# Kernel tuning notes

Hardware: AMD Instinct MI355X
Metric: run time of the kernel (lower is better)

The kernel has to match this reference:

```python
import jax, jax.numpy as jnp
import numpy as np

VOCAB = 128000
SEED = 0
PRIOR_TOKENS = 4
DEPTH = 16
TOP_P = 0.9


def setup_inputs() -> dict:
    key = jax.random.key(0)
    k1, k2 = jax.random.split(key)
    input_ids = jax.random.randint(k1, (32, 2048), 0, VOCAB, dtype=jnp.int64 if jax.config.jax_enable_x64 else jnp.int32)
    logits = jax.random.normal(k2, (32, VOCAB), dtype=jnp.float32)
    return {"input_ids": input_ids, "logits": logits}


def _g_values(prior_ids, depth, vocab):
    # Faithful structure: a deterministic Bernoulli(0.5) table of shape [B, depth, vocab]
    # seeded by (seed, prior_ids[b], depth_index). The original uses sha256+numpy RNG;
    # here we use the idiomatic JAX counterpart (fold_in keyed PRNG).
    base = jax.random.key(SEED)
    d_idx = jnp.arange(depth)

    def per_depth(k_b, i):
        return jax.random.bernoulli(jax.random.fold_in(k_b, i), 0.5, (vocab,))

    def per_batch(p):
        k_b = jax.random.fold_in(base, p.astype(jnp.uint32))
        return jax.vmap(lambda i: per_depth(k_b, i))(d_idx)

    return jax.vmap(per_batch)(prior_ids).astype(jnp.float32)  # [B, depth, V]


def _top_p_sample(probs_b, key, top_p):
    V = probs_b.shape[-1]
    sorted_probs, sorted_idx = jax.lax.top_k(probs_b, V)  # descending
    cum = jnp.cumsum(sorted_probs)
    cutoff = jnp.searchsorted(cum, top_p, side='left')
    keep = jnp.arange(V) <= cutoff  # zero out indices > cutoff (matches [cutoff+1:] = 0)
    sp = jnp.where(keep, sorted_probs, 0.0)
    sp = sp / sp.sum()
    sp = jnp.where(jnp.isfinite(sp), sp, 0.0)
    tok = jax.random.categorical(key, jnp.log(sp))  # multinomial(1)
    return sorted_idx[tok]


def reference(input_ids, logits):
    B, V = logits.shape
    prior_ids = input_ids[:, -PRIOR_TOKENS:].sum(axis=-1)  # [B]
    g = _g_values(prior_ids, DEPTH, V)                     # [B, depth, V]

    probs = jax.nn.softmax(logits, axis=-1)
    for i in range(DEPTH):
        g_i = g[:, i, :]                                   # [B, V]
        g_mass = jnp.sum(g_i * probs, axis=-1, keepdims=True)
        probs = probs * (1.0 + g_i - g_mass)

    sample_keys = jax.random.split(jax.random.key(SEED + 1), B)
    next_tokens = jax.vmap(lambda p, k: _top_p_sample(p, k, TOP_P))(probs, sample_keys)

    scores = jnp.full_like(logits, 1e-05)
    scores = scores.at[jnp.arange(B), next_tokens].set(100000.0)
    return scores
```

## Files before the change

kernel.cpp:

```cpp
#include <hip/hip_runtime.h>
#include <stdint.h>


#define NB 32
#define NV 128000
#define NDEPTH 16
#define NTB 500
#define NCB 125
#define NBINS 512
#define CAP 96256
#define NBLKH 94
#define FPSCALE 17592186044416.0
#define TSCALE  68719476736.0
#define MSCALE 1.152921504606846976e18

typedef unsigned long long u64;

__device__ __forceinline__ uint32_t rotl32(uint32_t v, int r) {
  return __builtin_amdgcn_alignbit(v, v, (32 - r) & 31);
}

__device__ __forceinline__ void tf2x32(uint32_t k0, uint32_t k1,
                                       uint32_t x0, uint32_t x1,
                                       uint32_t &o0, uint32_t &o1) {
  uint32_t ks2 = k0 ^ k1 ^ 0x1BD11BDAu;
  x0 += k0; x1 += k1;
  x0 += x1; x1 = rotl32(x1, 13); x1 ^= x0;
  x0 += x1; x1 = rotl32(x1, 15); x1 ^= x0;
  x0 += x1; x1 = rotl32(x1, 26); x1 ^= x0;
  x0 += x1; x1 = rotl32(x1,  6); x1 ^= x0;
  x0 += k1; x1 += ks2 + 1u;
  x0 += x1; x1 = rotl32(x1, 17); x1 ^= x0;
  x0 += x1; x1 = rotl32(x1, 29); x1 ^= x0;
  x0 += x1; x1 = rotl32(x1, 16); x1 ^= x0;
  x0 += x1; x1 = rotl32(x1, 24); x1 ^= x0;
  x0 += ks2; x1 += k0 + 2u;
  x0 += x1; x1 = rotl32(x1, 13); x1 ^= x0;
  x0 += x1; x1 = rotl32(x1, 15); x1 ^= x0;
  x0 += x1; x1 = rotl32(x1, 26); x1 ^= x0;
  x0 += x1; x1 = rotl32(x1,  6); x1 ^= x0;
  x0 += k0; x1 += k1 + 3u;
  x0 += x1; x1 = rotl32(x1, 17); x1 ^= x0;
  x0 += x1; x1 = rotl32(x1, 29); x1 ^= x0;
  x0 += x1; x1 = rotl32(x1, 16); x1 ^= x0;
  x0 += x1; x1 = rotl32(x1, 24); x1 ^= x0;
  x0 += k1; x1 += ks2 + 4u;
  x0 += x1; x1 = rotl32(x1, 13); x1 ^= x0;
  x0 += x1; x1 = rotl32(x1, 15); x1 ^= x0;
  x0 += x1; x1 = rotl32(x1, 26); x1 ^= x0;
  x0 += x1; x1 = rotl32(x1,  6); x1 ^= x0;
  x0 += ks2; x1 += k0 + 5u;
  o0 = x0; o1 = x1;
}

__device__ __forceinline__ uint32_t random_bits32(uint32_t k0, uint32_t k1, uint32_t i) {
  uint32_t y0, y1;
  tf2x32(k0, k1, 0u, i, y0, y1);
  return y0 ^ y1;
}

__global__ void keys_k(const int* __restrict__ ids, int T,
                       uint32_t* __restrict__ kd, uint32_t* __restrict__ sk) {
  int t = threadIdx.x;
  if (t >= NB) return;
  uint32_t prior = 0;
  for (int q = 0; q < 4; ++q) prior += (uint32_t)ids[(size_t)t * T + (T - 4) + q];
  uint32_t b0, b1;
  tf2x32(0u, 0u, 0u, prior, b0, b1);
  for (int d = 0; d < NDEPTH; ++d) {
    uint32_t y0, y1;
    tf2x32(b0, b1, 0u, (uint32_t)d, y0, y1);
    kd[(t * NDEPTH + d) * 2 + 0] = y0;
    kd[(t * NDEPTH + d) * 2 + 1] = y1;
  }
  uint32_t s0, s1;
  tf2x32(0u, 1u, 0u, (uint32_t)t, s0, s1);
  sk[2 * t + 0] = s0;
  sk[2 * t + 1] = s1;
}

__global__ void gmaskmax_k(const uint32_t* __restrict__ kd, const float* __restrict__ logits,
                           uint16_t* __restrict__ mask, float* __restrict__ pmax) {
  int blk = blockIdx.x, t = threadIdx.x;
  int b = blk / NTB, c = blk % NTB;
  uint32_t v = (uint32_t)(c * 256 + t);
  size_t i = (size_t)b * NV + v;
  const uint32_t* kp = kd + b * NDEPTH * 2;
  uint32_t m = 0;
  #pragma unroll
  for (int d = NDEPTH - 1; d >= 0; --d) {
    uint32_t k0 = __builtin_amdgcn_readfirstlane(kp[2 * d]);
    uint32_t k1 = __builtin_amdgcn_readfirstlane(kp[2 * d + 1]);
    uint32_t bits = random_bits32(k0, k1, v);
    m = (m << 1) | (bits >> 31);
  }
  mask[i] = (uint16_t)(m ^ 0xFFFFu);
  float x = logits[i];
  for (int o = 32; o > 0; o >>= 1) x = fmaxf(x, __shfl_xor(x, o));
  __shared__ float wmax[4];
  if ((t & 63) == 0) wmax[t >> 6] = x;
  __syncthreads();
  if (t == 0) pmax[b * NTB + c] = fmaxf(fmaxf(wmax[0], wmax[1]), fmaxf(wmax[2], wmax[3]));
}

__global__ void maxr2_k(const float* __restrict__ pmax, float* __restrict__ mx) {
  int t = threadIdx.x;
  int b = t >> 5, k = t & 31;
  float m = -3.4e38f;
  for (int i = k; i < NTB; i += 32) m = fmaxf(m, pmax[b * NTB + i]);
  for (int o = 16; o > 0; o >>= 1) m = fmaxf(m, __shfl_xor(m, o, 32));
  if (k == 0) mx[b] = m;
}

__global__ void lohist_k(const float* __restrict__ logits, const uint16_t* __restrict__ mask,
                         const float* __restrict__ mx, float* __restrict__ ef,
                         u64* __restrict__ Hlo) {
  int blk = blockIdx.x, t = threadIdx.x;
  int b = blk / NCB, c = blk % NCB;
  __shared__ u64 h[256];
  h[t] = 0ull;
  __syncthreads();
  float mxb = mx[b];
  size_t base = (size_t)b * NV + (size_t)c * 1024;
  #pragma unroll
  for (int e = 0; e < 4; ++e) {
    size_t i = base + e * 256 + t;
    float x = expf(logits[i] - mxb);
    ef[i] = x;
    atomicAdd(&h[mask[i] & 255u], (u64)((double)x * FPSCALE));
  }
  __syncthreads();
  if (h[t]) atomicAdd(&Hlo[b * 256 + t], h[t]);
}

__global__ void faclo_k(const u64* __restrict__ Hlo, u64* __restrict__ Zint,
                        float* __restrict__ zf, float* __restrict__ gm,
                        float* __restrict__ wloTab) {
  int b = blockIdx.x, t = threadIdx.x;
  u64 v = Hlo[b * 256 + t];
  __shared__ u64 zr[256];
  zr[t] = v; __syncthreads();
  for (int s = 128; s > 0; s >>= 1) { if (t < s) zr[t] += zr[t + s]; __syncthreads(); }
  __shared__ double Zsh;
  if (t == 0) {
    Zint[b] = zr[0];
    Zsh = (double)zr[0] * (1.0 / FPSCALE);
    zf[b] = (float)Zsh;
  }
  __syncthreads();
  double Zd = Zsh;
  float base = (float)((double)v * (1.0 / FPSCALE) / Zd);
  float w = 1.0f;
  __shared__ double dr[256];
  for (int d = 0; d < 8; ++d) {
    int bit = (t >> d) & 1;
    dr[t] = bit ? (double)(base * w) : 0.0;
    __syncthreads();
    for (int s = 128; s > 0; s >>= 1) { if (t < s) dr[t] += dr[t + s]; __syncthreads(); }
    float g = (float)dr[0];
    if (t == 0) gm[b * NDEPTH + d] = g;
    w *= (1.0f + (float)bit) - g;
    __syncthreads();
  }
  wloTab[b * 256 + t] = w;
}

__global__ void hihist_k(const float* __restrict__ ef, const uint16_t* __restrict__ mask,
                         const float* __restrict__ wloTab, u64* __restrict__ Thist) {
  int blk = blockIdx.x, t = threadIdx.x;
  int b = blk / NCB, c = blk % NCB;
  __shared__ u64 h[256];
  __shared__ float wl[256];
  h[t] = 0ull;
  wl[t] = wloTab[b * 256 + t];
  __syncthreads();
  size_t base = (size_t)b * NV + (size_t)c * 1024;
  #pragma unroll
  for (int e = 0; e < 4; ++e) {
    size_t i = base + e * 256 + t;
    uint32_t mk = mask[i];
    double prod = (double)ef[i] * (double)wl[mk & 255u];
    atomicAdd(&h[mk >> 8], (u64)(prod * TSCALE));
  }
  __syncthreads();
  if (h[t]) atomicAdd(&Thist[b * 256 + t], h[t]);
}

__global__ void fachi_k(const u64* __restrict__ Thist, const u64* __restrict__ Zint,
                        float* __restrict__ gm) {
  int b = blockIdx.x, t = threadIdx.x;
  double Zd = (double)Zint[b] * (1.0 / FPSCALE);
  u64 v = Thist[b * 256 + t];
  float base = (float)((double)v * (1.0 / TSCALE) / Zd);
  float w = 1.0f;
  __shared__ double dr[256];
  for (int d = 8; d < NDEPTH; ++d) {
    int bit = (t >> (d - 8)) & 1;
    dr[t] = bit ? (double)(base * w) : 0.0;
    __syncthreads();
    for (int s = 128; s > 0; s >>= 1) { if (t < s) dr[t] += dr[t + s]; __syncthreads(); }
    float g = (float)dr[0];
    if (t == 0) gm[b * NDEPTH + d] = g;
    w *= (1.0f + (float)bit) - g;
    __syncthreads();
  }
}

__global__ void final_k(float* __restrict__ efkeys, const uint16_t* __restrict__ mask,
                        const float* __restrict__ zf, const float* __restrict__ gm,
                        u64* __restrict__ binmass, uint32_t* __restrict__ bincnt) {
  int blk = blockIdx.x, t = threadIdx.x;
  int b = blk / NCB, c = blk % NCB;
  __shared__ float gsh[NDEPTH];
  __shared__ float zsh;
  __shared__ u64 bm[NBINS];
  __shared__ uint32_t bc[NBINS];
  if (t < NDEPTH) gsh[t] = gm[b * NDEPTH + t];
  if (t == 16) zsh = zf[b];
  for (int i = t; i < NBINS; i += 256) { bm[i] = 0ull; bc[i] = 0u; }
  __syncthreads();
  size_t base = (size_t)b * NV + (size_t)c * 1024;
  #pragma unroll
  for (int e = 0; e < 4; ++e) {
    size_t i = base + e * 256 + t;
    float p = efkeys[i] / zsh;
    uint16_t mk = mask[i];
    #pragma unroll
    for (int d = 0; d < NDEPTH; ++d) {
      float g = (float)((mk >> d) & 1);
      p = p * ((1.0f + g) - gsh[d]);
    }
    uint32_t key = ~__float_as_uint(p);
    ((uint32_t*)efkeys)[i] = key;
    uint32_t bin = key >> 23;
    atomicAdd(&bm[bin], (u64)((double)p * MSCALE));
    atomicAdd(&bc[bin], 1u);
  }
  __syncthreads();
  for (int k = t; k < NBINS; k += 256) {
    if (bc[k]) atomicAdd(&bincnt[b * NBINS + k], bc[k]);
    if (bm[k]) atomicAdd(&binmass[b * NBINS + k], bm[k]);
  }
}

__launch_bounds__(512)
__global__ void binsel_k(const u64* __restrict__ binmass, const uint32_t* __restrict__ bincnt,
                         uint32_t* __restrict__ Kthr, uint32_t* __restrict__ Hlen) {
  int b = blockIdx.x, t = threadIdx.x;
  __shared__ u64 cm[NBINS];
  __shared__ uint32_t cc[NBINS];
  __shared__ int selB;
  cm[t] = binmass[b * NBINS + t];
  cc[t] = bincnt[b * NBINS + t];
  if (t == 0) selB = NBINS - 2;
  __syncthreads();
  for (int off = 1; off < NBINS; off <<= 1) {
    u64 a = (t >= off) ? cm[t - off] : 0ull;
    uint32_t d = (t >= off) ? cc[t - off] : 0u;
    __syncthreads();
    cm[t] += a; cc[t] += d;
    __syncthreads();
  }
  const u64 thr = (u64)((double)0.9f * MSCALE);
  if (cm[t] >= thr && (t == 0 || cm[t - 1] < thr)) atomicMin(&selB, t);
  __syncthreads();
  if (t == 0) {
    int sb = selB;
    int margin = (cm[sb] >= thr && (cm[sb] - thr) > (1ull << 22)) ? 0 : 1;
    int Bs = sb + margin;
    if (Bs > NBINS - 1) Bs = NBINS - 1;
    while (Bs > 0 && cc[Bs] > CAP) --Bs;
    u64 kt = (((u64)(Bs + 1)) << 23) - 1ull;
    Kthr[b] = (uint32_t)kt;
    Hlen[b] = cc[Bs];
  }
}

__global__ void hcount_k(const uint32_t* __restrict__ keys, const uint32_t* __restrict__ Kthr,
                         uint32_t* __restrict__ hcnt) {
  int blk = blockIdx.x, t = threadIdx.x;
  int b = blk / NTB, c = blk % NTB;
  size_t i = (size_t)blk * 256 + t;
  bool active = keys[i] <= Kthr[b];
  u64 am = __ballot(active);
  __shared__ uint32_t wc[4];
  if ((t & 63) == 0) wc[t >> 6] = (uint32_t)__popcll(am);
  __syncthreads();
  if (t == 0) hcnt[b * NTB + c] = wc[0] + wc[1] + wc[2] + wc[3];
}

__launch_bounds__(1024)
__global__ void hscan_k(uint32_t* __restrict__ hcnt) {
  int b = blockIdx.x, t = threadIdx.x;
  uint32_t v = (t < NTB) ? hcnt[b * NTB + t] : 0u;
  __shared__ uint32_t sc[1024];
  sc[t] = v;
  __syncthreads();
  for (int off = 1; off < 1024; off <<= 1) {
    uint32_t a = (t >= off) ? sc[t - off] : 0u;
    __syncthreads();
    sc[t] += a;
    __syncthreads();
  }
  if (t < NTB) hcnt[b * NTB + t] = sc[t] - v;
}

__global__ void hcompact_k(const uint32_t* __restrict__ keys, const uint32_t* __restrict__ Kthr,
                           const uint32_t* __restrict__ hcnt, uint2* __restrict__ headA) {
  int blk = blockIdx.x, t = threadIdx.x;
  int b = blk / NTB, c = blk % NTB;
  int v = c * 256 + t;
  size_t i = (size_t)blk * 256 + t;
  uint32_t key = keys[i];
  bool active = key <= Kthr[b];
  int w = t >> 6, lane = t & 63;
  u64 am = __ballot(active);
  uint32_t rank = (uint32_t)__popcll(am & ((1ull << lane) - 1ull));
  __shared__ uint32_t wc[4];
  if ((t & 63) == 0) wc[t >> 6] = (uint32_t)__popcll(am);
  __syncthreads();
  uint32_t off = hcnt[b * NTB + c] + rank;
  for (int w2 = 0; w2 < w; ++w2) off += wc[w2];
  if (active) headA[(size_t)b * CAP + off] = make_uint2(key, (uint32_t)v);
}

__global__ void rhist_k(const uint2* __restrict__ src, const uint32_t* __restrict__ Hlen,
                        uint32_t* __restrict__ cnt, int shift) {
  int blk = blockIdx.x, t = threadIdx.x;
  int b = blk / NBLKH, c = blk % NBLKH;
  uint32_t H = Hlen[b];
  if ((uint32_t)(c * 1024) >= H) { cnt[((size_t)b * 256 + t) * NBLKH + c] = 0u; return; }
  const uint2* s = src + (size_t)b * CAP + (size_t)c * 1024;
  __shared__ uint32_t lh[256];
  lh[t] = 0;
  __syncthreads();
  #pragma unroll
  for (int e = 0; e < 4; ++e) {
    uint32_t idx = (uint32_t)(c * 1024 + 256 * e + t);
    if (idx < H) atomicAdd(&lh[(s[t + 256 * e].x >> shift) & 255u], 1u);
  }
  __syncthreads();
  cnt[((size_t)b * 256 + t) * NBLKH + c] = lh[t];
}

__launch_bounds__(1024)
__global__ void rscan_k(uint32_t* __restrict__ cnt) {
  const int NE = 256 * NBLKH;
  const int NL = 24;
  int b = blockIdx.x, t = threadIdx.x;
  uint32_t* cc = cnt + (size_t)b * NE;
  uint32_t loc[NL];
  uint32_t s = 0;
  int base = t * NL;
  #pragma unroll
  for (int j = 0; j < NL; ++j) {
    loc[j] = (base + j < NE) ? cc[base + j] : 0u;
    s += loc[j];
  }
  __shared__ uint32_t sc[1024];
  sc[t] = s;
  __syncthreads();
  for (int off = 1; off < 1024; off <<= 1) {
    uint32_t v = (t >= off) ? sc[t - off] : 0u;
    __syncthreads();
    sc[t] += v;
    __syncthreads();
  }
  uint32_t run = sc[t] - s;
  #pragma unroll
  for (int j = 0; j < NL; ++j) {
    if (base + j < NE) { uint32_t o = loc[j]; cc[base + j] = run; run += o; }
  }
}

__launch_bounds__(256)
__global__ void rscatter_k(const uint2* __restrict__ src, uint2* __restrict__ dst,
                           const uint32_t* __restrict__ Hlen,
                           const uint32_t* __restrict__ cnt, int shift) {
  int blk = blockIdx.x, t = threadIdx.x;
  int b = blk / NBLKH, c = blk % NBLKH;
  uint32_t H = Hlen[b];
  if ((uint32_t)(c * 1024) >= H) return;
  const uint2* s = src + (size_t)b * CAP + (size_t)c * 1024;
  uint2* d = dst + (size_t)b * CAP;
  int w = t >> 6, lane = t & 63;
  __shared__ uint32_t runb[256];
  __shared__ uint32_t wvc[4][256];
  runb[t] = cnt[((size_t)b * 256 + t) * NBLKH + c];
  uint2 el[4];
  #pragma unroll
  for (int e = 0; e < 4; ++e) el[e] = s[t + 256 * e];
  u64 lowmask = (1ull << lane) - 1ull;
  #pragma unroll
  for (int e = 0; e < 4; ++e) {
    uint32_t* wf = &wvc[0][0];
    wf[t] = 0; wf[t + 256] = 0; wf[t + 512] = 0; wf[t + 768] = 0;
    __syncthreads();
    bool active = (uint32_t)(c * 1024 + 256 * e + t) < H;
    uint32_t dig = active ? ((el[e].x >> shift) & 255u) : 0u;
    u64 act = __ballot(active);
    u64 m = ~0ull;
    #pragma unroll
    for (int bit = 0; bit < 8; ++bit) {
      u64 bb = __ballot((dig >> bit) & 1u);
      m &= ((dig >> bit) & 1u) ? bb : ~bb;
    }
    m &= act;
    uint32_t rank = (uint32_t)__popcll(m & lowmask);
    if (active && rank == 0) wvc[w][dig] = (uint32_t)__popcll(m);
    __syncthreads();
    if (active) {
      uint32_t off = runb[dig] + rank;
      for (int w2 = 0; w2 < w; ++w2) off += wvc[w2][dig];
      d[off] = el[e];
    }
    __syncthreads();
    runb[t] += wvc[0][t] + wvc[1][t] + wvc[2][t] + wvc[3][t];
    __syncthreads();
  }
}

__global__ void chunks_k(const uint2* __restrict__ sp, const uint32_t* __restrict__ Hlen,
                         double* __restrict__ cs) {
  int blk = blockIdx.x, t = threadIdx.x;
  int b = blk / NBLKH, c = blk % NBLKH;
  uint32_t H = Hlen[b];
  if ((uint32_t)(c * 1024) >= H) { if (t == 0) cs[b * NBLKH + c] = 0.0; return; }
  const uint2* p = sp + (size_t)b * CAP + (size_t)c * 1024;
  double s = 0.0;
  for (int k = t; k < 1024; k += 256) {
    uint32_t idx = (uint32_t)(c * 1024 + k);
    if (idx < H) s += (double)__uint_as_float(~p[k].x);
  }
  __shared__ double red[256];
  red[t] = s; __syncthreads();
  for (int st = 128; st > 0; st >>= 1) {
    if (t < st) red[t] += red[t + st];
    __syncthreads();
  }
  if (t == 0) cs[b * NBLKH + c] = red[0];
}

__launch_bounds__(1024)
__global__ void cutargmax_k(const uint2* __restrict__ sp, const double* __restrict__ cs,
                            const uint32_t* __restrict__ Hlen,
                            const uint32_t* __restrict__ sk, u64* __restrict__ best) {
  int b = blockIdx.x, t = threadIdx.x;
  const double TOPP = (double)0.9f;
  uint32_t H = Hlen[b];
  __shared__ double scd[1024];
  __shared__ int chSel;
  __shared__ double baseSel;
  __shared__ uint32_t cutSh;
  if (t == 0) { chSel = -1; baseSel = 0.0; cutSh = H - 1; }
  double v = (t < NBLKH) ? cs[b * NBLKH + t] : 0.0;
  scd[t] = v;
  __syncthreads();
  for (int off = 1; off < 1024; off <<= 1) {
    double a = (t >= off) ? scd[t - off] : 0.0;
    __syncthreads();
    scd[t] += a;
    __syncthreads();
  }
  if (t < NBLKH && scd[t] >= TOPP && (t == 0 || scd[t - 1] < TOPP)) {
    chSel = t;
    baseSel = (t == 0) ? 0.0 : scd[t - 1];
  }
  __syncthreads();
  int CH = chSel;
  if (CH >= 0) {
    double base = baseSel;
    uint32_t idx = (uint32_t)(CH * 1024 + t);
    double pv = (idx < H) ? (double)__uint_as_float(~sp[(size_t)b * CAP + idx].x) : 0.0;
    __syncthreads();
    scd[t] = pv;
    __syncthreads();
    for (int off = 1; off < 1024; off <<= 1) {
      double a = (t >= off) ? scd[t - off] : 0.0;
      __syncthreads();
      scd[t] += a;
      __syncthreads();
    }
    __shared__ int kSel;
    if (t == 0) kSel = 1023;
    __syncthreads();
    if (base + scd[t] >= TOPP && (t == 0 || base + scd[t - 1] < TOPP)) kSel = t;
    __syncthreads();
    if (t == 0) cutSh = (uint32_t)(CH * 1024 + kSel);
  }
  __syncthreads();
  uint32_t c = cutSh;
  uint32_t k0 = sk[2 * b], k1 = sk[2 * b + 1];
  u64 loc = 0ull;
  for (uint32_t j = (uint32_t)t; j <= c; j += 1024) {
    uint32_t bits = random_bits32(k0, k1, j);
    uint32_t m = bits >> 9;
    float u = (m == 0u) ? 1.17549435e-38f : (float)m * 1.1920928955078125e-7f;
    float gum = -logf(-logf(u));
    float scv = logf(__uint_as_float(~sp[(size_t)b * CAP + j].x)) + gum;
    uint32_t su = __float_as_uint(scv);
    uint32_t ord = (su & 0x80000000u) ? ~su : (su | 0x80000000u);
    u64 pk = ((u64)ord << 32) | (u64)(0xFFFFFFFFu - j);
    loc = (pk > loc) ? pk : loc;
  }
  __shared__ u64 redm[1024];
  redm[t] = loc;
  __syncthreads();
  for (int st = 512; st > 0; st >>= 1) {
    if (t < st) {
      u64 o = redm[t + st];
      if (o > redm[t]) redm[t] = o;
    }
    __syncthreads();
  }
  if (t == 0) best[b] = redm[0];
}

__global__ void fill_k(float* __restrict__ out) {
  size_t i = (size_t)blockIdx.x * 256 + threadIdx.x;
  out[i] = 1e-5f;
}

__global__ void win_k(const u64* __restrict__ best, const uint2* __restrict__ sp,
                      float* __restrict__ out) {
  int b = threadIdx.x;
  if (b >= NB) return;
  u64 pk = best[b];
  uint32_t j = 0xFFFFFFFFu - (uint32_t)(pk & 0xFFFFFFFFull);
  uint32_t tok = sp[(size_t)b * CAP + j].y;
  out[(size_t)b * NV + tok] = 100000.0f;
}

extern "C" void kernel_launch(void* const* d_in, const int* in_sizes, int n_in,
                              void* d_out, int out_size, void* d_ws, size_t ws_size,
                              hipStream_t stream) {
  const int* ids = (const int*)d_in[0];
  const float* logits = (const float*)d_in[1];
  float* out = (float*)d_out;
  int T = in_sizes[0] / NB;

  char* w = (char*)d_ws;
  uint2*    headA = (uint2*)(w + 0);
  uint2*    headB = (uint2*)(w + 24641536);
  uint16_t* mask  = (uint16_t*)(w + 49283072);
  float*    efkeys = (float*)(w + 24641536);
  uint32_t* keys   = (uint32_t*)(w + 24641536);
  uint32_t* cnt    = (uint32_t*)(w + 49283072);
  double*   csum   = (double*)(w + 52400000);
  char* S = w + 57475072;
  float*    pmax    = (float*)(S + 0);
  uint32_t* hcnt    = (uint32_t*)(S + 64000);
  float*    mx      = (float*)(S + 128000);
  float*    zf      = (float*)(S + 128128);
  float*    gm      = (float*)(S + 128256);
  uint32_t* kd      = (uint32_t*)(S + 130304);
  uint32_t* sk      = (uint32_t*)(S + 134400);
  u64*      best    = (u64*)(S + 134656);
  uint32_t* Kthr    = (uint32_t*)(S + 134912);
  uint32_t* Hlen    = (uint32_t*)(S + 135040);
  u64*      Zint    = (u64*)(S + 135168);
  float*    wloTab  = (float*)(S + 135424);
  char* ZR = S + 168192;
  u64*      Hlo     = (u64*)(ZR + 0);
  u64*      Thist   = (u64*)(ZR + 65536);
  u64*      binmass = (u64*)(ZR + 131072);
  uint32_t* bincnt  = (uint32_t*)(ZR + 262144);

  const int BVBLK = NB * NTB;
  const int CBLK  = NB * NCB;

  hipMemsetAsync(ZR, 0, 327680, stream);
  keys_k<<<1, 64, 0, stream>>>(ids, T, kd, sk);
  gmaskmax_k<<<BVBLK, 256, 0, stream>>>(kd, logits, mask, pmax);
  maxr2_k<<<1, 1024, 0, stream>>>(pmax, mx);
  lohist_k<<<CBLK, 256, 0, stream>>>(logits, mask, mx, efkeys, Hlo);
  faclo_k<<<NB, 256, 0, stream>>>(Hlo, Zint, zf, gm, wloTab);
  hihist_k<<<CBLK, 256, 0, stream>>>(efkeys, mask, wloTab, Thist);
  fachi_k<<<NB, 256, 0, stream>>>(Thist, Zint, gm);
  final_k<<<CBLK, 256, 0, stream>>>(efkeys, mask, zf, gm, binmass, bincnt);
  binsel_k<<<NB, NBINS, 0, stream>>>(binmass, bincnt, Kthr, Hlen);
  hcount_k<<<BVBLK, 256, 0, stream>>>(keys, Kthr, hcnt);
  hscan_k<<<NB, 1024, 0, stream>>>(hcnt);
  hcompact_k<<<BVBLK, 256, 0, stream>>>(keys, Kthr, hcnt, headA);

  const uint2* srcs[4] = { headA, headB, headA, headB };
  uint2*       dsts[4] = { headB, headA, headB, headA };
  for (int pass = 0; pass < 4; ++pass) {
    int shift = pass * 8;
    rhist_k<<<NB * NBLKH, 256, 0, stream>>>(srcs[pass], Hlen, cnt, shift);
    rscan_k<<<NB, 1024, 0, stream>>>(cnt);
    rscatter_k<<<NB * NBLKH, 256, 0, stream>>>(srcs[pass], dsts[pass], Hlen, cnt, shift);
  }

  chunks_k<<<NB * NBLKH, 256, 0, stream>>>(headA, Hlen, csum);
  cutargmax_k<<<NB, 1024, 0, stream>>>(headA, csum, Hlen, sk, best);
  fill_k<<<BVBLK, 256, 0, stream>>>(out);
  win_k<<<1, 32, 0, stream>>>(best, headA, out);
}
```

Baseline: 438.8 us.

## Fuse compaction into first radix pass, recompute exp, use wave-level scans

Several independent changes land together. The first radix pass now reads keys directly and filters them by threshold, which replaces the separate count/scan/compact kernels and removes one full radix pass. The exp(logit - max) values are recomputed in each kernel instead of being stored and reloaded, and the zeroing memset is folded into gmaskmax. Shared-memory Hillis-Steele scans and reductions in faclo, fachi, binsel, rscan and cutargmax become shuffle-based wave scans. This trades extra transcendental work and extra kernel complexity for fewer launches, passes and barriers.

```diff
diff --git a/kernel.cpp b/kernel.cpp
--- a/kernel.cpp
+++ b/kernel.cpp
@@ -80,19 +80,24 @@
 }
 
 __global__ void gmaskmax_k(const uint32_t* __restrict__ kd, const float* __restrict__ logits,
-                           uint16_t* __restrict__ mask, float* __restrict__ pmax) {
-  int blk = blockIdx.x, t = threadIdx.x;
+                           uint16_t* __restrict__ mask, float* __restrict__ pmax,
+                           uint32_t* __restrict__ ZR) {
+  int blk = blockIdx.x, t = threadIdx.x;
+  if (blk < 320) ZR[blk * 256 + t] = 0u;
   int b = blk / NTB, c = blk % NTB;
+  uint32_t K0[NDEPTH], K1[NDEPTH];
+  #pragma unroll
+  for (int d = 0; d < NDEPTH; ++d) {
+    K0[d] = kd[b * NDEPTH * 2 + 2 * d];
+    K1[d] = kd[b * NDEPTH * 2 + 2 * d + 1];
+  }
   uint32_t v = (uint32_t)(c * 256 + t);
   size_t i = (size_t)b * NV + v;
-  const uint32_t* kp = kd + b * NDEPTH * 2;
   uint32_t m = 0;
   #pragma unroll
   for (int d = NDEPTH - 1; d >= 0; --d) {
-    uint32_t k0 = __builtin_amdgcn_readfirstlane(kp[2 * d]);
-    uint32_t k1 = __builtin_amdgcn_readfirstlane(kp[2 * d + 1]);
-    uint32_t bits = random_bits32(k0, k1, v);
-    m = (m << 1) | (bits >> 31);
+    uint32_t bits = random_bits32(K0[d], K1[d], v);
+    m = __builtin_amdgcn_alignbit(m, bits, 31);
   }
   mask[i] = (uint16_t)(m ^ 0xFFFFu);
   float x = logits[i];
@@ -113,8 +118,7 @@
 }
 
 __global__ void lohist_k(const float* __restrict__ logits, const uint16_t* __restrict__ mask,
-                         const float* __restrict__ mx, float* __restrict__ ef,
-                         u64* __restrict__ Hlo) {
+                         const float* __restrict__ mx, u64* __restrict__ Hlo) {
   int blk = blockIdx.x, t = threadIdx.x;
   int b = blk / NCB, c = blk % NCB;
   __shared__ u64 h[256];
@@ -126,7 +130,6 @@
   for (int e = 0; e < 4; ++e) {
     size_t i = base + e * 256 + t;
     float x = expf(logits[i] - mxb);
-    ef[i] = x;
     atomicAdd(&h[mask[i] & 255u], (u64)((double)x * FPSCALE));
   }
   __syncthreads();
@@ -136,37 +139,42 @@
 __global__ void faclo_k(const u64* __restrict__ Hlo, u64* __restrict__ Zint,
                         float* __restrict__ zf, float* __restrict__ gm,
                         float* __restrict__ wloTab) {
-  int b = blockIdx.x, t = threadIdx.x;
-  u64 v = Hlo[b * 256 + t];
-  __shared__ u64 zr[256];
-  zr[t] = v; __syncthreads();
-  for (int s = 128; s > 0; s >>= 1) { if (t < s) zr[t] += zr[t + s]; __syncthreads(); }
-  __shared__ double Zsh;
-  if (t == 0) {
-    Zint[b] = zr[0];
-    Zsh = (double)zr[0] * (1.0 / FPSCALE);
-    zf[b] = (float)Zsh;
-  }
-  __syncthreads();
-  double Zd = Zsh;
-  float base = (float)((double)v * (1.0 / FPSCALE) / Zd);
-  float w = 1.0f;
-  __shared__ double dr[256];
+  int b = blockIdx.x, l = threadIdx.x;
+  u64 v[4];
+  #pragma unroll
+  for (int q = 0; q < 4; ++q) v[q] = Hlo[b * 256 + l + 64 * q];
+  u64 zp = v[0] + v[1] + v[2] + v[3];
+  for (int o = 32; o > 0; o >>= 1) zp += __shfl_xor(zp, o);
+  double Zd = (double)zp * (1.0 / FPSCALE);
+  if (l == 0) { Zint[b] = zp; zf[b] = (float)Zd; }
+  float base[4], w[4];
+  #pragma unroll
+  for (int q = 0; q < 4; ++q) {
+    base[q] = (float)((double)v[q] * (1.0 / FPSCALE) / Zd);
+    w[q] = 1.0f;
+  }
+  #pragma unroll
   for (int d = 0; d < 8; ++d) {
-    int bit = (t >> d) & 1;
-    dr[t] = bit ? (double)(base * w) : 0.0;
-    __syncthreads();
-    for (int s = 128; s > 0; s >>= 1) { if (t < s) dr[t] += dr[t + s]; __syncthreads(); }
-    float g = (float)dr[0];
-    if (t == 0) gm[b * NDEPTH + d] = g;
-    w *= (1.0f + (float)bit) - g;
-    __syncthreads();
-  }
-  wloTab[b * 256 + t] = w;
-}
-
-__global__ void hihist_k(const float* __restrict__ ef, const uint16_t* __restrict__ mask,
-                         const float* __restrict__ wloTab, u64* __restrict__ Thist) {
+    double part = 0.0;
+    #pragma unroll
+    for (int q = 0; q < 4; ++q)
+      if (((l + 64 * q) >> d) & 1) part += (double)(base[q] * w[q]);
+    for (int o = 32; o > 0; o >>= 1) part += __shfl_xor(part, o);
+    float g = (float)part;
+    if (l == 0) gm[b * NDEPTH + d] = g;
+    #pragma unroll
+    for (int q = 0; q < 4; ++q) {
+      int bit = ((l + 64 * q) >> d) & 1;
+      w[q] *= (1.0f + (float)bit) - g;
+    }
+  }
+  #pragma unroll
+  for (int q = 0; q < 4; ++q) wloTab[b * 256 + l + 64 * q] = w[q];
+}
+
+__global__ void hihist_k(const float* __restrict__ logits, const uint16_t* __restrict__ mask,
+                         const float* __restrict__ mx, const float* __restrict__ wloTab,
+                         u64* __restrict__ Thist) {
   int blk = blockIdx.x, t = threadIdx.x;
   int b = blk / NCB, c = blk % NCB;
   __shared__ u64 h[256];
@@ -174,12 +182,14 @@
   h[t] = 0ull;
   wl[t] = wloTab[b * 256 + t];
   __syncthreads();
+  float mxb = mx[b];
   size_t base = (size_t)b * NV + (size_t)c * 1024;
   #pragma unroll
   for (int e = 0; e < 4; ++e) {
     size_t i = base + e * 256 + t;
+    float x = expf(logits[i] - mxb);
     uint32_t mk = mask[i];
-    double prod = (double)ef[i] * (double)wl[mk & 255u];
+    double prod = (double)x * (double)wl[mk & 255u];
     atomicAdd(&h[mk >> 8], (u64)(prod * TSCALE));
   }
   __syncthreads();
@@ -188,42 +198,54 @@
 
 __global__ void fachi_k(const u64* __restrict__ Thist, const u64* __restrict__ Zint,
                         float* __restrict__ gm) {
-  int b = blockIdx.x, t = threadIdx.x;
+  int b = blockIdx.x, l = threadIdx.x;
   double Zd = (double)Zint[b] * (1.0 / FPSCALE);
-  u64 v = Thist[b * 256 + t];
-  float base = (float)((double)v * (1.0 / TSCALE) / Zd);
-  float w = 1.0f;
-  __shared__ double dr[256];
+  u64 v[4];
+  #pragma unroll
+  for (int q = 0; q < 4; ++q) v[q] = Thist[b * 256 + l + 64 * q];
+  float base[4], w[4];
+  #pragma unroll
+  for (int q = 0; q < 4; ++q) {
+    base[q] = (float)((double)v[q] * (1.0 / TSCALE) / Zd);
+    w[q] = 1.0f;
+  }
+  #pragma unroll
   for (int d = 8; d < NDEPTH; ++d) {
-    int bit = (t >> (d - 8)) & 1;
-    dr[t] = bit ? (double)(base * w) : 0.0;
-    __syncthreads();
-    for (int s = 128; s > 0; s >>= 1) { if (t < s) dr[t] += dr[t + s]; __syncthreads(); }
-    float g = (float)dr[0];
-    if (t == 0) gm[b * NDEPTH + d] = g;
-    w *= (1.0f + (float)bit) - g;
-    __syncthreads();
-  }
-}
-
-__global__ void final_k(float* __restrict__ efkeys, const uint16_t* __restrict__ mask,
-                        const float* __restrict__ zf, const float* __restrict__ gm,
+    double part = 0.0;
+    #pragma unroll
+    for (int q = 0; q < 4; ++q)
+      if (((l + 64 * q) >> (d - 8)) & 1) part += (double)(base[q] * w[q]);
+    for (int o = 32; o > 0; o >>= 1) part += __shfl_xor(part, o);
+    float g = (float)part;
+    if (l == 0) gm[b * NDEPTH + d] = g;
+    #pragma unroll
+    for (int q = 0; q < 4; ++q) {
+      int bit = ((l + 64 * q) >> (d - 8)) & 1;
+      w[q] *= (1.0f + (float)bit) - g;
+    }
+  }
+}
+
+__global__ void final_k(const float* __restrict__ logits, const uint16_t* __restrict__ mask,
+                        const float* __restrict__ mx, const float* __restrict__ zf,
+                        const float* __restrict__ gm, uint32_t* __restrict__ keys,
                         u64* __restrict__ binmass, uint32_t* __restrict__ bincnt) {
   int blk = blockIdx.x, t = threadIdx.x;
   int b = blk / NCB, c = blk % NCB;
   __shared__ float gsh[NDEPTH];
-  __shared__ float zsh;
+  __shared__ float zsh, msh;
   __shared__ u64 bm[NBINS];
   __shared__ uint32_t bc[NBINS];
   if (t < NDEPTH) gsh[t] = gm[b * NDEPTH + t];
   if (t == 16) zsh = zf[b];
+  if (t == 17) msh = mx[b];
   for (int i = t; i < NBINS; i += 256) { bm[i] = 0ull; bc[i] = 0u; }
   __syncthreads();
   size_t base = (size_t)b * NV + (size_t)c * 1024;
   #pragma unroll
   for (int e = 0; e < 4; ++e) {
     size_t i = base + e * 256 + t;
-    float p = efkeys[i] / zsh;
+    float p = expf(logits[i] - msh) / zsh;
     uint16_t mk = mask[i];
     #pragma unroll
     for (int d = 0; d < NDEPTH; ++d) {
@@ -231,7 +253,7 @@
       p = p * ((1.0f + g) - gsh[d]);
     }
     uint32_t key = ~__float_as_uint(p);
-    ((uint32_t*)efkeys)[i] = key;
+    keys[i] = key;
     uint32_t bin = key >> 23;
     atomicAdd(&bm[bin], (u64)((double)p * MSCALE));
     atomicAdd(&bc[bin], 1u);
@@ -243,85 +265,152 @@
   }
 }
 
-__launch_bounds__(512)
 __global__ void binsel_k(const u64* __restrict__ binmass, const uint32_t* __restrict__ bincnt,
                          uint32_t* __restrict__ Kthr, uint32_t* __restrict__ Hlen) {
-  int b = blockIdx.x, t = threadIdx.x;
-  __shared__ u64 cm[NBINS];
-  __shared__ uint32_t cc[NBINS];
-  __shared__ int selB;
-  cm[t] = binmass[b * NBINS + t];
-  cc[t] = bincnt[b * NBINS + t];
-  if (t == 0) selB = NBINS - 2;
-  __syncthreads();
-  for (int off = 1; off < NBINS; off <<= 1) {
-    u64 a = (t >= off) ? cm[t - off] : 0ull;
-    uint32_t d = (t >= off) ? cc[t - off] : 0u;
-    __syncthreads();
-    cm[t] += a; cc[t] += d;
-    __syncthreads();
-  }
+  int b = blockIdx.x, l = threadIdx.x;
+  u64 m[8]; uint32_t c[8];
+  #pragma unroll
+  for (int r = 0; r < 8; ++r) {
+    m[r] = binmass[b * NBINS + l * 8 + r];
+    c[r] = bincnt[b * NBINS + l * 8 + r];
+  }
+  #pragma unroll
+  for (int r = 1; r < 8; ++r) { m[r] += m[r - 1]; c[r] += c[r - 1]; }
+  u64 lm = m[7]; uint32_t lc = c[7];
+  u64 im = lm; uint32_t ic = lc;
+  for (int o = 1; o < 64; o <<= 1) {
+    u64 nm = __shfl_up(im, o);
+    uint32_t nc = __shfl_up(ic, o);
+    if (l >= o) { im += nm; ic += nc; }
+  }
+  u64 baseM = im - lm;
+  uint32_t baseC = ic - lc;
+  __shared__ uint32_t ccL[NBINS];
+  #pragma unroll
+  for (int r = 0; r < 8; ++r) ccL[l * 8 + r] = baseC + c[r];
   const u64 thr = (u64)((double)0.9f * MSCALE);
-  if (cm[t] >= thr && (t == 0 || cm[t - 1] < thr)) atomicMin(&selB, t);
-  __syncthreads();
-  if (t == 0) {
-    int sb = selB;
-    int margin = (cm[sb] >= thr && (cm[sb] - thr) > (1ull << 22)) ? 0 : 1;
-    int Bs = sb + margin;
+  int localFirst = 8; u64 cmAt = 0ull;
+  #pragma unroll
+  for (int r = 0; r < 8; ++r) {
+    if (localFirst == 8 && baseM + m[r] >= thr) { localFirst = r; cmAt = baseM + m[r]; }
+  }
+  u64 bal = __ballot(localFirst < 8);
+  int selB = NBINS - 2; u64 cmSel = 0ull;
+  if (bal) {
+    int fl = __ffsll((unsigned long long)bal) - 1;
+    int sl = __shfl(localFirst, fl);
+    cmSel = __shfl(cmAt, fl);
+    selB = fl * 8 + sl;
+  }
+  __syncthreads();
+  if (l == 0) {
+    int margin = (cmSel >= thr && (cmSel - thr) > (1ull << 22)) ? 0 : 1;
+    int Bs = selB + margin;
     if (Bs > NBINS - 1) Bs = NBINS - 1;
-    while (Bs > 0 && cc[Bs] > CAP) --Bs;
-    u64 kt = (((u64)(Bs + 1)) << 23) - 1ull;
-    Kthr[b] = (uint32_t)kt;
-    Hlen[b] = cc[Bs];
-  }
-}
-
-__global__ void hcount_k(const uint32_t* __restrict__ keys, const uint32_t* __restrict__ Kthr,
-                         uint32_t* __restrict__ hcnt) {
-  int blk = blockIdx.x, t = threadIdx.x;
-  int b = blk / NTB, c = blk % NTB;
-  size_t i = (size_t)blk * 256 + t;
-  bool active = keys[i] <= Kthr[b];
-  u64 am = __ballot(active);
-  __shared__ uint32_t wc[4];
-  if ((t & 63) == 0) wc[t >> 6] = (uint32_t)__popcll(am);
-  __syncthreads();
-  if (t == 0) hcnt[b * NTB + c] = wc[0] + wc[1] + wc[2] + wc[3];
-}
-
+    while (Bs > 0 && ccL[Bs] > CAP) --Bs;
+    Kthr[b] = (uint32_t)((((u64)(Bs + 1)) << 23) - 1ull);
+    Hlen[b] = ccL[Bs];
+  }
+}
+
+template<int NCH, int NL>
 __launch_bounds__(1024)
-__global__ void hscan_k(uint32_t* __restrict__ hcnt) {
-  int b = blockIdx.x, t = threadIdx.x;
-  uint32_t v = (t < NTB) ? hcnt[b * NTB + t] : 0u;
-  __shared__ uint32_t sc[1024];
-  sc[t] = v;
-  __syncthreads();
-  for (int off = 1; off < 1024; off <<= 1) {
-    uint32_t a = (t >= off) ? sc[t - off] : 0u;
-    __syncthreads();
-    sc[t] += a;
-    __syncthreads();
-  }
-  if (t < NTB) hcnt[b * NTB + t] = sc[t] - v;
-}
-
-__global__ void hcompact_k(const uint32_t* __restrict__ keys, const uint32_t* __restrict__ Kthr,
-                           const uint32_t* __restrict__ hcnt, uint2* __restrict__ headA) {
-  int blk = blockIdx.x, t = threadIdx.x;
-  int b = blk / NTB, c = blk % NTB;
-  int v = c * 256 + t;
-  size_t i = (size_t)blk * 256 + t;
-  uint32_t key = keys[i];
-  bool active = key <= Kthr[b];
+__global__ void rscan_t(uint32_t* __restrict__ cnt) {
+  const int NE = 256 * NCH;
+  int b = blockIdx.x, t = threadIdx.x, l = t & 63, wv = t >> 6;
+  uint32_t* cc = cnt + (size_t)b * NE;
+  uint32_t loc[NL];
+  uint32_t s = 0;
+  int base = t * NL;
+  #pragma unroll
+  for (int j = 0; j < NL; ++j) {
+    loc[j] = (base + j < NE) ? cc[base + j] : 0u;
+    s += loc[j];
+  }
+  uint32_t incl = s;
+  for (int o = 1; o < 64; o <<= 1) {
+    uint32_t n = __shfl_up(incl, o);
+    if (l >= o) incl += n;
+  }
+  __shared__ uint32_t wtot[16], wbase[16];
+  if (l == 63) wtot[wv] = incl;
+  __syncthreads();
+  if (t < 16) {
+    uint32_t v = wtot[t], i2 = v;
+    for (int o = 1; o < 16; o <<= 1) {
+      uint32_t n = __shfl_up(i2, o);
+      if (t >= o) i2 += n;
+    }
+    wbase[t] = i2 - v;
+  }
+  __syncthreads();
+  uint32_t run = wbase[wv] + (incl - s);
+  #pragma unroll
+  for (int j = 0; j < NL; ++j) {
+    if (base + j < NE) { uint32_t o = loc[j]; cc[base + j] = run; run += o; }
+  }
+}
+
+__global__ void rhist1_k(const uint32_t* __restrict__ keys, const uint32_t* __restrict__ Kthr,
+                         uint32_t* __restrict__ cnt) {
+  int blk = blockIdx.x, t = threadIdx.x;
+  int b = blk / NCB, c = blk % NCB;
+  uint32_t KT = Kthr[b];
+  __shared__ uint32_t lh[256];
+  lh[t] = 0;
+  __syncthreads();
+  size_t base = (size_t)b * NV + (size_t)c * 1024;
+  #pragma unroll
+  for (int e = 0; e < 4; ++e) {
+    uint32_t k = keys[base + 256 * e + t];
+    if (k <= KT) atomicAdd(&lh[k & 255u], 1u);
+  }
+  __syncthreads();
+  cnt[((size_t)b * 256 + t) * NCB + c] = lh[t];
+}
+
+__launch_bounds__(256)
+__global__ void rscatter1_k(const uint32_t* __restrict__ keys, const uint32_t* __restrict__ Kthr,
+                            const uint32_t* __restrict__ cnt, uint2* __restrict__ dst0) {
+  int blk = blockIdx.x, t = threadIdx.x;
+  int b = blk / NCB, c = blk % NCB;
+  uint32_t KT = Kthr[b];
+  uint2* d = dst0 + (size_t)b * CAP;
   int w = t >> 6, lane = t & 63;
-  u64 am = __ballot(active);
-  uint32_t rank = (uint32_t)__popcll(am & ((1ull << lane) - 1ull));
-  __shared__ uint32_t wc[4];
-  if ((t & 63) == 0) wc[t >> 6] = (uint32_t)__popcll(am);
-  __syncthreads();
-  uint32_t off = hcnt[b * NTB + c] + rank;
-  for (int w2 = 0; w2 < w; ++w2) off += wc[w2];
-  if (active) headA[(size_t)b * CAP + off] = make_uint2(key, (uint32_t)v);
+  __shared__ uint32_t runb[256];
+  __shared__ uint32_t wvc[4][256];
+  runb[t] = cnt[((size_t)b * 256 + t) * NCB + c];
+  size_t base = (size_t)b * NV + (size_t)c * 1024;
+  uint32_t el[4];
+  #pragma unroll
+  for (int e = 0; e < 4; ++e) el[e] = keys[base + 256 * e + t];
+  u64 lowmask = (1ull << lane) - 1ull;
+  #pragma unroll
+  for (int e = 0; e < 4; ++e) {
+    wvc[0][t] = 0; wvc[1][t] = 0; wvc[2][t] = 0; wvc[3][t] = 0;
+    __syncthreads();
+    bool active = el[e] <= KT;
+    uint32_t dig = active ? (el[e] & 255u) : 0u;
+    u64 act = __ballot(active);
+    u64 m = ~0ull;
+    #pragma unroll
+    for (int bit = 0; bit < 8; ++bit) {
+      u64 bb = __ballot((dig >> bit) & 1u);
+      m &= ((dig >> bit) & 1u) ? bb : ~bb;
+    }
+    m &= act;
+    uint32_t rank = (uint32_t)__popcll(m & lowmask);
+    if (active && rank == 0) wvc[w][dig] = (uint32_t)__popcll(m);
+    __syncthreads();
+    if (active) {
+      uint32_t off = runb[dig] + rank;
+      for (int w2 = 0; w2 < w; ++w2) off += wvc[w2][dig];
+      d[off] = make_uint2(el[e], (uint32_t)(c * 1024 + 256 * e + t));
+    }
+    __syncthreads();
+    runb[t] += wvc[0][t] + wvc[1][t] + wvc[2][t] + wvc[3][t];
+    __syncthreads();
+  }
 }
 
 __global__ void rhist_k(const uint2* __restrict__ src, const uint32_t* __restrict__ Hlen,
@@ -341,36 +430,6 @@
   }
   __syncthreads();
   cnt[((size_t)b * 256 + t) * NBLKH + c] = lh[t];
-}
-
-__launch_bounds__(1024)
-__global__ void rscan_k(uint32_t* __restrict__ cnt) {
-  const int NE = 256 * NBLKH;
-  const int NL = 24;
-  int b = blockIdx.x, t = threadIdx.x;
-  uint32_t* cc = cnt + (size_t)b * NE;
-  uint32_t loc[NL];
-  uint32_t s = 0;
-  int base = t * NL;
-  #pragma unroll
-  for (int j = 0; j < NL; ++j) {
-    loc[j] = (base + j < NE) ? cc[base + j] : 0u;
-    s += loc[j];
-  }
-  __shared__ uint32_t sc[1024];
-  sc[t] = s;
-  __syncthreads();
-  for (int off = 1; off < 1024; off <<= 1) {
-    uint32_t v = (t >= off) ? sc[t - off] : 0u;
-    __syncthreads();
-    sc[t] += v;
-    __syncthreads();
-  }
-  uint32_t run = sc[t] - s;
-  #pragma unroll
-  for (int j = 0; j < NL; ++j) {
-    if (base + j < NE) { uint32_t o = loc[j]; cc[base + j] = run; run += o; }
-  }
 }
 
 __launch_bounds__(256)
@@ -393,8 +452,7 @@
   u64 lowmask = (1ull << lane) - 1ull;
   #pragma unroll
   for (int e = 0; e < 4; ++e) {
-    uint32_t* wf = &wvc[0][0];
-    wf[t] = 0; wf[t + 256] = 0; wf[t + 512] = 0; wf[t + 768] = 0;
+    wvc[0][t] = 0; wvc[1][t] = 0; wvc[2][t] = 0; wvc[3][t] = 0;
     __syncthreads();
     bool active = (uint32_t)(c * 1024 + 256 * e + t) < H;
     uint32_t dig = active ? ((el[e].x >> shift) & 255u) : 0u;
@@ -445,51 +503,64 @@
 __global__ void cutargmax_k(const uint2* __restrict__ sp, const double* __restrict__ cs,
                             const uint32_t* __restrict__ Hlen,
                             const uint32_t* __restrict__ sk, u64* __restrict__ best) {
-  int b = blockIdx.x, t = threadIdx.x;
+  int b = blockIdx.x, t = threadIdx.x, l = t & 63, wv = t >> 6;
   const double TOPP = (double)0.9f;
   uint32_t H = Hlen[b];
-  __shared__ double scd[1024];
-  __shared__ int chSel;
-  __shared__ double baseSel;
-  __shared__ uint32_t cutSh;
-  if (t == 0) { chSel = -1; baseSel = 0.0; cutSh = H - 1; }
-  double v = (t < NBLKH) ? cs[b * NBLKH + t] : 0.0;
-  scd[t] = v;
-  __syncthreads();
-  for (int off = 1; off < 1024; off <<= 1) {
-    double a = (t >= off) ? scd[t - off] : 0.0;
-    __syncthreads();
-    scd[t] += a;
-    __syncthreads();
-  }
-  if (t < NBLKH && scd[t] >= TOPP && (t == 0 || scd[t - 1] < TOPP)) {
-    chSel = t;
-    baseSel = (t == 0) ? 0.0 : scd[t - 1];
-  }
-  __syncthreads();
-  int CH = chSel;
+  __shared__ double sh_base;
+  __shared__ int sh_ch;
+  __shared__ uint32_t sh_cut;
+  __shared__ double wsum[16];
+  __shared__ u64 wmx[16];
+  __shared__ int kSel;
+  if (t == 0) { sh_ch = -1; sh_base = 0.0; sh_cut = H - 1; kSel = 1023; }
+  __syncthreads();
+  if (wv == 0) {
+    double v0 = (l < NBLKH) ? cs[b * NBLKH + l] : 0.0;
+    double v1 = (l + 64 < NBLKH) ? cs[b * NBLKH + l + 64] : 0.0;
+    double i0 = v0;
+    for (int o = 1; o < 64; o <<= 1) { double n = __shfl_up(i0, o); if (l >= o) i0 += n; }
+    double T0 = __shfl(i0, 63);
+    double i1 = v1;
+    for (int o = 1; o < 64; o <<= 1) { double n = __shfl_up(i1, o); if (l >= o) i1 += n; }
+    i1 += T0;
+    bool h0 = (l < NBLKH) && (i0 >= TOPP);
+    bool h1 = (l + 64 < NBLKH) && (i1 >= TOPP);
+    u64 b0m = __ballot(h0);
+    u64 b1m = __ballot(h1);
+    int ch = -1; double bse = 0.0;
+    if (b0m) {
+      int fl = __ffsll((unsigned long long)b0m) - 1;
+      ch = fl; bse = __shfl(i0, fl) - __shfl(v0, fl);
+    } else if (b1m) {
+      int fl = __ffsll((unsigned long long)b1m) - 1;
+      ch = 64 + fl; bse = __shfl(i1, fl) - __shfl(v1, fl);
+    }
+    if (l == 0) { sh_ch = ch; sh_base = bse; }
+  }
+  __syncthreads();
+  int CH = sh_ch;
   if (CH >= 0) {
-    double base = baseSel;
+    double base = sh_base;
     uint32_t idx = (uint32_t)(CH * 1024 + t);
     double pv = (idx < H) ? (double)__uint_as_float(~sp[(size_t)b * CAP + idx].x) : 0.0;
-    __syncthreads();
-    scd[t] = pv;
-    __syncthreads();
-    for (int off = 1; off < 1024; off <<= 1) {
-      double a = (t >= off) ? scd[t - off] : 0.0;
-      __syncthreads();
-      scd[t] += a;
-      __syncthreads();
-    }
-    __shared__ int kSel;
-    if (t == 0) kSel = 1023;
-    __syncthreads();
-    if (base + scd[t] >= TOPP && (t == 0 || base + scd[t - 1] < TOPP)) kSel = t;
-    __syncthreads();
-    if (t == 0) cutSh = (uint32_t)(CH * 1024 + kSel);
-  }
-  __syncthreads();
-  uint32_t c = cutSh;
+    double iv = pv;
+    for (int o = 1; o < 64; o <<= 1) { double n = __shfl_up(iv, o); if (l >= o) iv += n; }
+    if (l == 63) wsum[wv] = iv;
+    __syncthreads();
+    if (t < 16) {
+      double v = wsum[t], i2 = v;
+      for (int o = 1; o < 16; o <<= 1) { double n = __shfl_up(i2, o); if (t >= o) i2 += n; }
+      wsum[t] = i2 - v;
+    }
+    __syncthreads();
+    double full = base + wsum[wv] + iv;
+    double prev = full - pv;
+    if (full >= TOPP && prev < TOPP) atomicMin(&kSel, (int)t);
+    __syncthreads();
+    if (t == 0) sh_cut = (uint32_t)(CH * 1024 + (kSel < 1024 ? kSel : 1023));
+  }
+  __syncthreads();
+  uint32_t c = sh_cut;
   uint32_t k0 = sk[2 * b], k1 = sk[2 * b + 1];
   u64 loc = 0ull;
   for (uint32_t j = (uint32_t)t; j <= c; j += 1024) {
@@ -503,17 +574,17 @@
     u64 pk = ((u64)ord << 32) | (u64)(0xFFFFFFFFu - j);
     loc = (pk > loc) ? pk : loc;
   }
-  __shared__ u64 redm[1024];
-  redm[t] = loc;
-  __syncthreads();
-  for (int st = 512; st > 0; st >>= 1) {
-    if (t < st) {
-      u64 o = redm[t + st];
-      if (o > redm[t]) redm[t] = o;
-    }
-    __syncthreads();
-  }
-  if (t == 0) best[b] = redm[0];
+  for (int o = 32; o > 0; o >>= 1) {
+    u64 oth = __shfl_xor(loc, o);
+    loc = (oth > loc) ? oth : loc;
+  }
+  if (l == 0) wmx[wv] = loc;
+  __syncthreads();
+  if (t == 0) {
+    u64 m = wmx[0];
+    for (int k = 1; k < 16; ++k) m = (wmx[k] > m) ? wmx[k] : m;
+    best[b] = m;
+  }
 }
 
 __global__ void fill_k(float* __restrict__ out) {
@@ -542,25 +613,23 @@
   char* w = (char*)d_ws;
   uint2*    headA = (uint2*)(w + 0);
   uint2*    headB = (uint2*)(w + 24641536);
-  uint16_t* mask  = (uint16_t*)(w + 49283072);
-  float*    efkeys = (float*)(w + 24641536);
-  uint32_t* keys   = (uint32_t*)(w + 24641536);
-  uint32_t* cnt    = (uint32_t*)(w + 49283072);
-  double*   csum   = (double*)(w + 52400000);
-  char* S = w + 57475072;
+  uint32_t* keys  = (uint32_t*)(w + 24641536);
+  uint32_t* cnt   = (uint32_t*)(w + 49283072);
+  uint16_t* mask  = (uint16_t*)(w + 53379072);
+  char* S = w + 61571072;
   float*    pmax    = (float*)(S + 0);
-  uint32_t* hcnt    = (uint32_t*)(S + 64000);
-  float*    mx      = (float*)(S + 128000);
-  float*    zf      = (float*)(S + 128128);
-  float*    gm      = (float*)(S + 128256);
-  uint32_t* kd      = (uint32_t*)(S + 130304);
-  uint32_t* sk      = (uint32_t*)(S + 134400);
-  u64*      best    = (u64*)(S + 134656);
-  uint32_t* Kthr    = (uint32_t*)(S + 134912);
-  uint32_t* Hlen    = (uint32_t*)(S + 135040);
-  u64*      Zint    = (u64*)(S + 135168);
-  float*    wloTab  = (float*)(S + 135424);
-  char* ZR = S + 168192;
+  double*   csum    = (double*)(S + 64000);
+  float*    mx      = (float*)(S + 88064);
+  float*    zf      = (float*)(S + 88192);
+  float*    gm      = (float*)(S + 88320);
+  uint32_t* Kthr    = (uint32_t*)(S + 90368);
+  uint32_t* Hlen    = (uint32_t*)(S + 90496);
+  u64*      Zint    = (u64*)(S + 90624);
+  float*    wloTab  = (float*)(S + 90880);
+  u64*      best    = (u64*)(S + 123648);
+  uint32_t* kd      = (uint32_t*)(S + 123904);
+  uint32_t* sk      = (uint32_t*)(S + 128000);
+  char* ZR = S + 128256;
   u64*      Hlo     = (u64*)(ZR + 0);
   u64*      Thist   = (u64*)(ZR + 65536);
   u64*      binmass = (u64*)(ZR + 131072);
@@ -569,31 +638,31 @@
   const int BVBLK = NB * NTB;
   const int CBLK  = NB * NCB;
 
-  hipMemsetAsync(ZR, 0, 327680, stream);
   keys_k<<<1, 64, 0, stream>>>(ids, T, kd, sk);
-  gmaskmax_k<<<BVBLK, 256, 0, stream>>>(kd, logits, mask, pmax);
+  gmaskmax_k<<<BVBLK, 256, 0, stream>>>(kd, logits, mask, pmax, (uint32_t*)ZR);
   maxr2_k<<<1, 1024, 0, stream>>>(pmax, mx);
-  lohist_k<<<CBLK, 256, 0, stream>>>(logits, mask, mx, efkeys, Hlo);
-  faclo_k<<<NB, 256, 0, stream>>>(Hlo, Zint, zf, gm, wloTab);
-  hihist_k<<<CBLK, 256, 0, stream>>>(efkeys, mask, wloTab, Thist);
-  fachi_k<<<NB, 256, 0, stream>>>(Thist, Zint, gm);
-  final_k<<<CBLK, 256, 0, stream>>>(efkeys, mask, zf, gm, binmass, bincnt);
-  binsel_k<<<NB, NBINS, 0, stream>>>(binmass, bincnt, Kthr, Hlen);
-  hcount_k<<<BVBLK, 256, 0, stream>>>(keys, Kthr, hcnt);
-  hscan_k<<<NB, 1024, 0, stream>>>(hcnt);
-  hcompact_k<<<BVBLK, 256, 0, stream>>>(keys, Kthr, hcnt, headA);
-
-  const uint2* srcs[4] = { headA, headB, headA, headB };
-  uint2*       dsts[4] = { headB, headA, headB, headA };
-  for (int pass = 0; pass < 4; ++pass) {
-    int shift = pass * 8;
+  lohist_k<<<CBLK, 256, 0, stream>>>(logits, mask, mx, Hlo);
+  faclo_k<<<NB, 64, 0, stream>>>(Hlo, Zint, zf, gm, wloTab);
+  hihist_k<<<CBLK, 256, 0, stream>>>(logits, mask, mx, wloTab, Thist);
+  fachi_k<<<NB, 64, 0, stream>>>(Thist, Zint, gm);
+  final_k<<<CBLK, 256, 0, stream>>>(logits, mask, mx, zf, gm, keys, binmass, bincnt);
+  binsel_k<<<NB, 64, 0, stream>>>(binmass, bincnt, Kthr, Hlen);
+
+  rhist1_k<<<CBLK, 256, 0, stream>>>(keys, Kthr, cnt);
+  rscan_t<NCB, 32><<<NB, 1024, 0, stream>>>(cnt);
+  rscatter1_k<<<CBLK, 256, 0, stream>>>(keys, Kthr, cnt, headA);
+
+  const uint2* srcs[3] = { headA, headB, headA };
+  uint2*       dsts[3] = { headB, headA, headB };
+  for (int pass = 0; pass < 3; ++pass) {
+    int shift = (pass + 1) * 8;
     rhist_k<<<NB * NBLKH, 256, 0, stream>>>(srcs[pass], Hlen, cnt, shift);
-    rscan_k<<<NB, 1024, 0, stream>>>(cnt);
+    rscan_t<NBLKH, 24><<<NB, 1024, 0, stream>>>(cnt);
     rscatter_k<<<NB * NBLKH, 256, 0, stream>>>(srcs[pass], dsts[pass], Hlen, cnt, shift);
   }
 
-  chunks_k<<<NB * NBLKH, 256, 0, stream>>>(headA, Hlen, csum);
-  cutargmax_k<<<NB, 1024, 0, stream>>>(headA, csum, Hlen, sk, best);
+  chunks_k<<<NB * NBLKH, 256, 0, stream>>>(headB, Hlen, csum);
+  cutargmax_k<<<NB, 1024, 0, stream>>>(headB, csum, Hlen, sk, best);
   fill_k<<<BVBLK, 256, 0, stream>>>(out);
-  win_k<<<1, 32, 0, stream>>>(best, headA, out);
-}
+  win_k<<<1, 32, 0, stream>>>(best, headB, out);
+}
```

Measured after the change: 419.7 us. 1.05x faster.
